# Performance work log

Measured on AMD Instinct MI355X. Metric: run time of the kernel, lower is better.

Reference implementation:

```python
import jax, jax.numpy as jnp
import numpy as np

B, T, V, E, U = 1024, 256, 50000, 512, 1024

def setup_inputs() -> dict:
    key = jax.random.key(0)
    ks = jax.random.split(key, 10)
    s = lambda k, shape, fan: jax.random.normal(k, shape, dtype=jnp.float32) * (1.0 / np.sqrt(fan))
    return {
        "inputs": jax.random.randint(ks[0], (B, T), 0, V, dtype=jnp.int32),
        "emb": s(ks[1], (V, E), E),
        "W0": s(ks[2], (E, U), E),
        "U0": s(ks[3], (U, U), U),
        "b0": jnp.zeros((U,), jnp.float32),
        "W1": s(ks[4], (U, U), U),
        "U1": s(ks[5], (U, U), U),
        "b1": jnp.zeros((U,), jnp.float32),
        "Wout": s(ks[6], (U, 1), U),
        "bout": jnp.zeros((1,), jnp.float32),
    }

def reference(inputs, emb, W0, U0, b0, W1, U1, b1, Wout, bout):
    x = emb[inputs]                      # [B, T, E] embedding lookup
    xT = jnp.swapaxes(x, 0, 1)           # [T, B, E] time-major for scan
    h0_init = jnp.zeros((inputs.shape[0], U0.shape[0]), x.dtype)
    h1_init = jnp.zeros((inputs.shape[0], U1.shape[0]), x.dtype)

    def step(carry, xt):
        h0, h1 = carry
        h0 = jnp.tanh(xt @ W0 + h0 @ U0 + b0)   # SimpleRNNCell 0 (dropout inactive, inference)
        h1 = jnp.tanh(h0 @ W1 + h1 @ U1 + b1)   # SimpleRNNCell 1
        return (h0, h1), None

    (h0, h1), _ = jax.lax.scan(step, (h0_init, h1_init), xT)
    return jax.nn.sigmoid(h1 @ Wout + bout)      # [B, 1]
```

## Files before the change

kernel.cpp:

```cpp
#include <hip/hip_runtime.h>
#include <hip/hip_cooperative_groups.h>
#include <math.h>

namespace cg = cooperative_groups;

typedef unsigned short u16;
typedef __bf16 bf16x8 __attribute__((ext_vector_type(8)));
typedef float f32x4 __attribute__((ext_vector_type(4)));
typedef unsigned short u16x8 __attribute__((ext_vector_type(8)));
typedef int i32x4 __attribute__((ext_vector_type(4)));

#define NBLK 256
#define NTHR 256
#define BB 1024
#define TT 256
#define EE 512
#define UU 1024
#define K0 1536
#define K1 2048
#define NK0 48
#define NK1 64
#define KTL0 32
#define KTL1 16
#define HN0 ((size_t)BB * K0)
#define HN1 ((size_t)BB * K1)
#define LDS_BYTES 163840

#define ROSTER_BASE 0
#define FLAG_BASE 32
#define EPOCH_BASE (32 + 2048)
#define BAR_INTS 2560

#define AUX_SC0 1

__device__ i32x4 llvm_amdgcn_raw_buffer_load_i32x4(i32x4 srsrc, int voffset, int soffset,
                                                   int aux) __asm("llvm.amdgcn.raw.buffer.load.v4i32");

__device__ __forceinline__ i32x4 make_srd(const void* p) {
  union { const void* p; int i[2]; } u; u.p = p;
  i32x4 r; r.x = u.i[0]; r.y = u.i[1]; r.z = -1; r.w = 0x00020000;
  return r;
}

__device__ __forceinline__ u16 f2bf(float f) {
  unsigned u = __builtin_bit_cast(unsigned, f);
  u += 0x7fffu + ((u >> 16) & 1u);
  return (u16)(u >> 16);
}
__device__ __forceinline__ float bf2f(u16 h) {
  return __builtin_bit_cast(float, ((unsigned)h) << 16);
}
__device__ __forceinline__ float fast_tanh(float x) {
  x = fminf(fmaxf(x, -15.f), 15.f);
  float e = __expf(2.f * x);
  return (e - 1.f) / (e + 1.f);
}

template<int K, int KLOW>
__device__ __forceinline__ void wfill(u16* __restrict__ Wt,
    const float* __restrict__ Wl, const float* __restrict__ Wh, int gstart) {
  constexpr int NK = K / 32;
  constexpr int NG = 1024 * K / 8;
  for (int g = gstart; g < NG; g += NBLK * NTHR) {
    const int lane = g & 63;
    const int r = g >> 6;
    const int kt = r % NK;
    const int cb = r / NK;
    const int n = cb * 16 + (lane & 15);
    const int kb = kt * 32 + (lane >> 4) * 8;
    u16x8 o;
#pragma unroll
    for (int e = 0; e < 8; ++e) {
      const int k = kb + e;
      const float v = (k < KLOW) ? Wl[(size_t)k * UU + n] : Wh[(size_t)(k - KLOW) * UU + n];
      o[e] = f2bf(v);
    }
    *(u16x8*)(Wt + (size_t)g * 8) = o;
  }
}

__device__ __forceinline__ void xbar(int* __restrict__ bar, int xcc, int slot, int nx,
                                     int tgt, int tid) {
  __syncthreads();
  if (tid < 64) {
    if (tid == 0)
      __hip_atomic_store(&bar[FLAG_BASE + xcc * 256 + slot], tgt,
                         __ATOMIC_RELAXED, __HIP_MEMORY_SCOPE_AGENT);
    if (slot == 0) {
      for (int base = 0; base < nx; base += 64) {
        const int i = base + tid;
        const bool act = (i < nx);
        int guard = 0;
        bool done = false;
        do {
          int v = act ? __hip_atomic_load(&bar[FLAG_BASE + xcc * 256 + i],
                                          __ATOMIC_RELAXED, __HIP_MEMORY_SCOPE_AGENT)
                      : tgt;
          done = __all(v >= tgt) != 0;
        } while (!done && ++guard < 300000);
      }
      if (tid == 0)
        __hip_atomic_store(&bar[EPOCH_BASE + xcc * 32], tgt,
                           __ATOMIC_RELAXED, __HIP_MEMORY_SCOPE_AGENT);
    } else if (tid == 0) {
      int guard = 0;
      while (__hip_atomic_load(&bar[EPOCH_BASE + xcc * 32],
                               __ATOMIC_RELAXED, __HIP_MEMORY_SCOPE_AGENT) < tgt
             && ++guard < 600000)
        __builtin_amdgcn_s_sleep(8);
    }
  }
  __syncthreads();
}

template<int K>
__device__ __forceinline__ void kstep(const i32x4& srdA, int voA, int kt,
    const u16* __restrict__ p0, const u16* __restrict__ p1,
    const u16* __restrict__ p2, const u16* __restrict__ p3,
    int lo, f32x4 (&acc)[2][4]) {
  i32x4 a0 = llvm_amdgcn_raw_buffer_load_i32x4(srdA, voA + kt * 64, 0, AUX_SC0);
  i32x4 a1 = llvm_amdgcn_raw_buffer_load_i32x4(srdA, voA + 16 * K * 2 + kt * 64, 0, AUX_SC0);
  u16x8 b0 = *(const u16x8*)(p0 + (size_t)kt * 512 + lo);
  u16x8 b1 = *(const u16x8*)(p1 + (size_t)kt * 512 + lo);
  u16x8 b2 = *(const u16x8*)(p2 + (size_t)kt * 512 + lo);
  u16x8 b3 = *(const u16x8*)(p3 + (size_t)kt * 512 + lo);
  bf16x8 fa0 = __builtin_bit_cast(bf16x8, a0);
  bf16x8 fa1 = __builtin_bit_cast(bf16x8, a1);
  bf16x8 fb0 = __builtin_bit_cast(bf16x8, b0);
  bf16x8 fb1 = __builtin_bit_cast(bf16x8, b1);
  bf16x8 fb2 = __builtin_bit_cast(bf16x8, b2);
  bf16x8 fb3 = __builtin_bit_cast(bf16x8, b3);
  acc[0][0] = __builtin_amdgcn_mfma_f32_16x16x32_bf16(fa0, fb0, acc[0][0], 0, 0, 0);
  acc[0][1] = __builtin_amdgcn_mfma_f32_16x16x32_bf16(fa0, fb1, acc[0][1], 0, 0, 0);
  acc[0][2] = __builtin_amdgcn_mfma_f32_16x16x32_bf16(fa0, fb2, acc[0][2], 0, 0, 0);
  acc[0][3] = __builtin_amdgcn_mfma_f32_16x16x32_bf16(fa0, fb3, acc[0][3], 0, 0, 0);
  acc[1][0] = __builtin_amdgcn_mfma_f32_16x16x32_bf16(fa1, fb0, acc[1][0], 0, 0, 0);
  acc[1][1] = __builtin_amdgcn_mfma_f32_16x16x32_bf16(fa1, fb1, acc[1][1], 0, 0, 0);
  acc[1][2] = __builtin_amdgcn_mfma_f32_16x16x32_bf16(fa1, fb2, acc[1][2], 0, 0, 0);
  acc[1][3] = __builtin_amdgcn_mfma_f32_16x16x32_bf16(fa1, fb3, acc[1][3], 0, 0, 0);
}

template<int K, int KTL>
__device__ __forceinline__ void gemm2(const i32x4& srdA, int voA,
    const u16* __restrict__ bA, const u16* __restrict__ bB,
    const u16* __restrict__ bP, int lane, f32x4 (&acc)[2][4]) {
  constexpr int NK = K / 32;
  const int lo = lane * 8;
  const u16* p0 = bA;
  const u16* p1 = bA + (size_t)NK * 512;
#pragma unroll 8
  for (int kt = 0; kt < KTL; ++kt)
    kstep<K>(srdA, voA, kt, p0, p1, bP, bP + (size_t)KTL * 512, lo, acc);
#pragma unroll 8
  for (int kt = KTL; kt < NK; ++kt)
    kstep<K>(srdA, voA, kt, p0, p1, bB, bB + (size_t)NK * 512, lo, acc);
}

__device__ __forceinline__ void do_l0(int tk, int xcc, int jl, bool uselds,
    const u16* __restrict__ ldsb, const u16* __restrict__ Wt0,
    const int* __restrict__ inputs, const float* __restrict__ emb,
    const float* __restrict__ b0, u16* __restrict__ A0, u16* __restrict__ A1,
    int tid)
{
  const int lane = tid & 63, w = tid >> 6, q = lane >> 4, l16 = lane & 15;
  const int c0 = jl * 64;
  if (tk < TT - 1) {
    const int grow = xcc * 128 + jl * 8 + (tid >> 5);
    const int c = (tid & 31) * 16;
    const int idx = inputs[grow * TT + tk + 1];
    const f32x4* s = (const f32x4*)(emb + (size_t)idx * EE + c);
    f32x4 f0 = s[0], f1 = s[1], f2 = s[2], f3 = s[3];
    u16x8 oa, ob;
#pragma unroll
    for (int j = 0; j < 4; ++j) {
      oa[j] = f2bf(f0[j]); oa[j + 4] = f2bf(f1[j]);
      ob[j] = f2bf(f2[j]); ob[j + 4] = f2bf(f3[j]);
    }
    u16* dst = A0 + (size_t)((tk + 1) & 1) * HN0 + (size_t)grow * K0 + c;
    *(u16x8*)dst = oa;
    *(u16x8*)(dst + 8) = ob;
  }
  if (tk < TT) {
    f32x4 acc[2][4];
#pragma unroll
    for (int i = 0; i < 2; ++i)
#pragma unroll
      for (int n = 0; n < 4; ++n) acc[i][n] = (f32x4){0.f, 0.f, 0.f, 0.f};
    i32x4 srdA = make_srd(A0 + (size_t)(tk & 1) * HN0);
    const int voA = ((xcc * 128 + w * 32 + l16) * K0 + q * 8) * 2;
    const u16* gA = Wt0 + (size_t)(c0 / 16) * NK0 * 512;
    const u16* bB = Wt0 + (size_t)(c0 / 16 + 2) * NK0 * 512;
    if (uselds) gemm2<K0, KTL0>(srdA, voA, ldsb, bB,
                                ldsb + (size_t)2 * NK0 * 512, lane, acc);
    else        gemm2<K0, 0   >(srdA, voA, gA, bB, ldsb, lane, acc);
    u16* d1 = A1 + (size_t)(tk & 1) * HN1;
    u16* d2 = A0 + (size_t)((tk + 1) & 1) * HN0 + 512;
#pragma unroll
    for (int n = 0; n < 4; ++n) {
      const int col = c0 + n * 16 + l16;
      const float bs = b0[col];
#pragma unroll
      for (int i = 0; i < 2; ++i) {
#pragma unroll
        for (int rr = 0; rr < 4; ++rr) {
          const int grow = xcc * 128 + w * 32 + i * 16 + q * 4 + rr;
          const u16 v = f2bf(fast_tanh(acc[i][n][rr] + bs));
          d1[(size_t)grow * K1 + col] = v;
          d2[(size_t)grow * K0 + col] = v;
        }
      }
    }
  }
}

__device__ __forceinline__ void do_l1(int tk, int xcc, int jl, bool uselds,
    const u16* __restrict__ ldsb, const u16* __restrict__ Wt1,
    const float* __restrict__ b1, u16* __restrict__ A1, int tid)
{
  const int lane = tid & 63, w = tid >> 6, q = lane >> 4, l16 = lane & 15;
  const int c0 = jl * 64;
  f32x4 acc[2][4];
#pragma unroll
  for (int i = 0; i < 2; ++i)
#pragma unroll
    for (int n = 0; n < 4; ++n) acc[i][n] = (f32x4){0.f, 0.f, 0.f, 0.f};
  i32x4 srdA = make_srd(A1 + (size_t)((tk - 1) & 1) * HN1);
  const int voA = ((xcc * 128 + w * 32 + l16) * K1 + q * 8) * 2;
  const u16* gA = Wt1 + (size_t)(c0 / 16) * NK1 * 512;
  const u16* bB = Wt1 + (size_t)(c0 / 16 + 2) * NK1 * 512;
  if (uselds) gemm2<K1, KTL1>(srdA, voA, ldsb, bB,
                              ldsb + (size_t)2 * NK1 * 512, lane, acc);
  else        gemm2<K1, 0   >(srdA, voA, gA, bB, ldsb, lane, acc);
  u16* d1 = A1 + (size_t)(tk & 1) * HN1 + 1024;
#pragma unroll
  for (int n = 0; n < 4; ++n) {
    const int col = c0 + n * 16 + l16;
    const float bs = b1[col];
#pragma unroll
    for (int i = 0; i < 2; ++i) {
#pragma unroll
      for (int rr = 0; rr < 4; ++rr) {
        const int grow = xcc * 128 + w * 32 + i * 16 + q * 4 + rr;
        d1[(size_t)grow * K1 + col] = f2bf(fast_tanh(acc[i][n][rr] + bs));
      }
    }
  }
}

__global__ __launch_bounds__(NTHR, 1)
void rnn_kernel(const int* __restrict__ inputs, const float* __restrict__ emb,
    const float* __restrict__ W0, const float* __restrict__ U0, const float* __restrict__ b0,
    const float* __restrict__ W1, const float* __restrict__ U1, const float* __restrict__ b1,
    const float* __restrict__ Wout, const float* __restrict__ bout,
    float* __restrict__ out,
    u16* __restrict__ Wt0, u16* __restrict__ Wt1,
    u16* __restrict__ A0, u16* __restrict__ A1, int* __restrict__ bar)
{
  extern __shared__ u16 lds[];
  int* li = (int*)lds;
  cg::grid_group grid = cg::this_grid();
  const int tid = threadIdx.x, bid = blockIdx.x;

  const int gstart = bid * NTHR + tid;
  wfill<K0, 512>(Wt0, W0, U0, gstart);
  wfill<K1, 1024>(Wt1, W1, U1, gstart);
  for (int g = gstart; g < BB * EE / 8; g += NBLK * NTHR) {
    const int b = g >> 6, seg = g & 63;
    const int idx = inputs[b * TT];
    const f32x4* s = (const f32x4*)(emb + (size_t)idx * EE + seg * 8);
    f32x4 f0 = s[0], f1 = s[1];
    u16x8 o;
#pragma unroll
    for (int j = 0; j < 4; ++j) { o[j] = f2bf(f0[j]); o[j + 4] = f2bf(f1[j]); }
    *(u16x8*)(A0 + (size_t)b * K0 + seg * 8) = o;
  }
  {
    const u16x8 z = {0, 0, 0, 0, 0, 0, 0, 0};
    for (int g = gstart; g < BB * 1024 / 8; g += NBLK * NTHR) {
      const int b = g >> 7, seg = g & 127;
      *(u16x8*)(A0 + (size_t)b * K0 + 512 + seg * 8) = z;
      *(u16x8*)(A1 + (size_t)b * K1 + 1024 + seg * 8) = z;
    }
  }
  if (bid == 0) for (int i = tid; i < BAR_INTS; i += NTHR) bar[i] = 0;
  grid.sync();

  if (tid == 0) {
    const int xc = __builtin_amdgcn_s_getreg((7 << 11) | 20) & 7;
    li[0] = xc;
    li[1] = atomicAdd(&bar[ROSTER_BASE + xc], 1);
  }
  __syncthreads();
  const int xcc = li[0], slot = li[1];
  __syncthreads();
  grid.sync();
  if (tid == 0)
    li[0] = __hip_atomic_load(&bar[ROSTER_BASE + xcc],
                              __ATOMIC_RELAXED, __HIP_MEMORY_SCOPE_AGENT);
  __syncthreads();
  const int nx = li[0];
  __syncthreads();

  if (slot < 32) {
    const bool pL0 = slot < 16;
    const int cb = (pL0 ? slot : slot - 16) * 4;
    const int NKp = pL0 ? NK0 : NK1;
    const int KTLp = pL0 ? KTL0 : KTL1;
    const u16* W = pL0 ? Wt0 : Wt1;
    const u16x8* s = (const u16x8*)(W + (size_t)cb * NKp * 512);
    const int nv = 2 * NKp * 64;
    u16x8* d = (u16x8*)lds;
    for (int i = tid; i < nv; i += NTHR) d[i] = s[i];
    u16x8* d2 = d + nv;
    const int nv2 = 2 * KTLp * 64;
    for (int i = tid; i < nv2; i += NTHR) {
      const int f = i / (KTLp * 64);
      const int rem = i - f * (KTLp * 64);
      d2[i] = *((const u16x8*)(W + (size_t)(cb + 2 + f) * NKp * 512) + rem);
    }
  }
  __syncthreads();

  for (int tk = 0; tk <= TT; ++tk) {
    for (int job = slot; job < 32; job += nx) {
      const bool uselds = (job == slot);
      if (job < 16) do_l0(tk, xcc, job, uselds, lds, Wt0, inputs, emb, b0, A0, A1, tid);
      else if (tk >= 1) do_l1(tk, xcc, job - 16, uselds, lds, Wt1, b1, A1, tid);
    }
    xbar(bar, xcc, slot, nx, tk + 1, tid);
  }

  if (slot == 0) {
    const int lane = tid & 63, w = tid >> 6;
    i32x4 srdH = make_srd(A1);
    const f32x4* wv = (const f32x4*)(Wout + lane * 16);
    f32x4 w0 = wv[0], w1 = wv[1], w2 = wv[2], w3 = wv[3];
    for (int rr = 0; rr < 32; ++rr) {
      const int grow = xcc * 128 + w * 32 + rr;
      const int vo = (grow * K1 + 1024 + lane * 16) * 2;
      i32x4 hv0 = llvm_amdgcn_raw_buffer_load_i32x4(srdH, vo, 0, AUX_SC0);
      i32x4 hv1 = llvm_amdgcn_raw_buffer_load_i32x4(srdH, vo + 16, 0, AUX_SC0);
      u16x8 lo = __builtin_bit_cast(u16x8, hv0);
      u16x8 hi = __builtin_bit_cast(u16x8, hv1);
      float s = 0.f;
#pragma unroll
      for (int j = 0; j < 4; ++j) {
        s += bf2f(lo[j]) * w0[j];
        s += bf2f(lo[j + 4]) * w1[j];
        s += bf2f(hi[j]) * w2[j];
        s += bf2f(hi[j + 4]) * w3[j];
      }
#pragma unroll
      for (int off = 32; off > 0; off >>= 1) s += __shfl_down(s, off);
      if (lane == 0) out[grow] = 1.f / (1.f + expf(-(s + bout[0])));
    }
  }
}

extern "C" void kernel_launch(void* const* d_in, const int* in_sizes, int n_in,
                              void* d_out, int out_size, void* d_ws, size_t ws_size,
                              hipStream_t stream)
{
  (void)in_sizes; (void)n_in; (void)out_size; (void)ws_size;
  const int*   inputs = (const int*)d_in[0];
  const float* emb    = (const float*)d_in[1];
  const float* W0     = (const float*)d_in[2];
  const float* U0     = (const float*)d_in[3];
  const float* b0     = (const float*)d_in[4];
  const float* W1     = (const float*)d_in[5];
  const float* U1     = (const float*)d_in[6];
  const float* b1     = (const float*)d_in[7];
  const float* Wout   = (const float*)d_in[8];
  const float* bout   = (const float*)d_in[9];
  float* out = (float*)d_out;

  u16* Wt0 = (u16*)d_ws;
  u16* Wt1 = Wt0 + (size_t)1024 * K0;
  u16* A0  = Wt1 + (size_t)1024 * K1;
  u16* A1  = A0 + (size_t)2 * 1024 * K0;
  int* bar = (int*)(A1 + (size_t)2 * 1024 * K1);

  static int lds_set = 0;
  if (!lds_set) {
    hipFuncSetAttribute((const void*)rnn_kernel,
                        hipFuncAttributeMaxDynamicSharedMemorySize, LDS_BYTES);
    lds_set = 1;
  }

  void* args[] = { &inputs, &emb, &W0, &U0, &b0, &W1, &U1, &b1, &Wout, &bout,
                   &out, &Wt0, &Wt1, &A0, &A1, &bar };
  hipLaunchCooperativeKernel((void*)rnn_kernel, dim3(NBLK), dim3(NTHR), args, LDS_BYTES, stream);
}
```

Measured before the change: 7.214 ms.

## Double block threads to 512, each wave computing 16 rows instead of 32

Raises the block size from 256 to 512 threads, so each of 8 waves computes a 16-row by 64-column tile instead of a 32x64 tile. The A-fragment load and half the MFMAs per k-step move to the extra waves, and the embedding staging and output reduction are reindexed to match. This raises per-CU wave parallelism and latency hiding for the per-timestep GEMMs. The cost is that each B fragment, read from LDS or global memory, is now loaded by twice as many waves for half as much reuse, and register pressure per wave changes under launch_bounds(512,1).

```diff
diff --git a/kernel.cpp b/kernel.cpp
--- a/kernel.cpp
+++ b/kernel.cpp
@@ -11,7 +11,7 @@
 typedef int i32x4 __attribute__((ext_vector_type(4)));
 
 #define NBLK 256
-#define NTHR 256
+#define NTHR 512
 #define BB 1024
 #define TT 256
 #define EE 512
@@ -117,33 +117,27 @@
 __device__ __forceinline__ void kstep(const i32x4& srdA, int voA, int kt,
     const u16* __restrict__ p0, const u16* __restrict__ p1,
     const u16* __restrict__ p2, const u16* __restrict__ p3,
-    int lo, f32x4 (&acc)[2][4]) {
+    int lo, f32x4 (&acc)[4]) {
   i32x4 a0 = llvm_amdgcn_raw_buffer_load_i32x4(srdA, voA + kt * 64, 0, AUX_SC0);
-  i32x4 a1 = llvm_amdgcn_raw_buffer_load_i32x4(srdA, voA + 16 * K * 2 + kt * 64, 0, AUX_SC0);
   u16x8 b0 = *(const u16x8*)(p0 + (size_t)kt * 512 + lo);
   u16x8 b1 = *(const u16x8*)(p1 + (size_t)kt * 512 + lo);
   u16x8 b2 = *(const u16x8*)(p2 + (size_t)kt * 512 + lo);
   u16x8 b3 = *(const u16x8*)(p3 + (size_t)kt * 512 + lo);
   bf16x8 fa0 = __builtin_bit_cast(bf16x8, a0);
-  bf16x8 fa1 = __builtin_bit_cast(bf16x8, a1);
   bf16x8 fb0 = __builtin_bit_cast(bf16x8, b0);
   bf16x8 fb1 = __builtin_bit_cast(bf16x8, b1);
   bf16x8 fb2 = __builtin_bit_cast(bf16x8, b2);
   bf16x8 fb3 = __builtin_bit_cast(bf16x8, b3);
-  acc[0][0] = __builtin_amdgcn_mfma_f32_16x16x32_bf16(fa0, fb0, acc[0][0], 0, 0, 0);
-  acc[0][1] = __builtin_amdgcn_mfma_f32_16x16x32_bf16(fa0, fb1, acc[0][1], 0, 0, 0);
-  acc[0][2] = __builtin_amdgcn_mfma_f32_16x16x32_bf16(fa0, fb2, acc[0][2], 0, 0, 0);
-  acc[0][3] = __builtin_amdgcn_mfma_f32_16x16x32_bf16(fa0, fb3, acc[0][3], 0, 0, 0);
-  acc[1][0] = __builtin_amdgcn_mfma_f32_16x16x32_bf16(fa1, fb0, acc[1][0], 0, 0, 0);
-  acc[1][1] = __builtin_amdgcn_mfma_f32_16x16x32_bf16(fa1, fb1, acc[1][1], 0, 0, 0);
-  acc[1][2] = __builtin_amdgcn_mfma_f32_16x16x32_bf16(fa1, fb2, acc[1][2], 0, 0, 0);
-  acc[1][3] = __builtin_amdgcn_mfma_f32_16x16x32_bf16(fa1, fb3, acc[1][3], 0, 0, 0);
+  acc[0] = __builtin_amdgcn_mfma_f32_16x16x32_bf16(fa0, fb0, acc[0], 0, 0, 0);
+  acc[1] = __builtin_amdgcn_mfma_f32_16x16x32_bf16(fa0, fb1, acc[1], 0, 0, 0);
+  acc[2] = __builtin_amdgcn_mfma_f32_16x16x32_bf16(fa0, fb2, acc[2], 0, 0, 0);
+  acc[3] = __builtin_amdgcn_mfma_f32_16x16x32_bf16(fa0, fb3, acc[3], 0, 0, 0);
 }
 
 template<int K, int KTL>
 __device__ __forceinline__ void gemm2(const i32x4& srdA, int voA,
     const u16* __restrict__ bA, const u16* __restrict__ bB,
-    const u16* __restrict__ bP, int lane, f32x4 (&acc)[2][4]) {
+    const u16* __restrict__ bP, int lane, f32x4 (&acc)[4]) {
   constexpr int NK = K / 32;
   const int lo = lane * 8;
   const u16* p0 = bA;
@@ -165,29 +159,22 @@
   const int lane = tid & 63, w = tid >> 6, q = lane >> 4, l16 = lane & 15;
   const int c0 = jl * 64;
   if (tk < TT - 1) {
-    const int grow = xcc * 128 + jl * 8 + (tid >> 5);
-    const int c = (tid & 31) * 16;
+    const int grow = xcc * 128 + jl * 8 + (tid >> 6);
+    const int c = (tid & 63) * 8;
     const int idx = inputs[grow * TT + tk + 1];
     const f32x4* s = (const f32x4*)(emb + (size_t)idx * EE + c);
-    f32x4 f0 = s[0], f1 = s[1], f2 = s[2], f3 = s[3];
-    u16x8 oa, ob;
-#pragma unroll
-    for (int j = 0; j < 4; ++j) {
-      oa[j] = f2bf(f0[j]); oa[j + 4] = f2bf(f1[j]);
-      ob[j] = f2bf(f2[j]); ob[j + 4] = f2bf(f3[j]);
-    }
-    u16* dst = A0 + (size_t)((tk + 1) & 1) * HN0 + (size_t)grow * K0 + c;
-    *(u16x8*)dst = oa;
-    *(u16x8*)(dst + 8) = ob;
+    f32x4 f0 = s[0], f1 = s[1];
+    u16x8 oa;
+#pragma unroll
+    for (int j = 0; j < 4; ++j) { oa[j] = f2bf(f0[j]); oa[j + 4] = f2bf(f1[j]); }
+    *(u16x8*)(A0 + (size_t)((tk + 1) & 1) * HN0 + (size_t)grow * K0 + c) = oa;
   }
   if (tk < TT) {
-    f32x4 acc[2][4];
-#pragma unroll
-    for (int i = 0; i < 2; ++i)
-#pragma unroll
-      for (int n = 0; n < 4; ++n) acc[i][n] = (f32x4){0.f, 0.f, 0.f, 0.f};
+    f32x4 acc[4];
+#pragma unroll
+    for (int n = 0; n < 4; ++n) acc[n] = (f32x4){0.f, 0.f, 0.f, 0.f};
     i32x4 srdA = make_srd(A0 + (size_t)(tk & 1) * HN0);
-    const int voA = ((xcc * 128 + w * 32 + l16) * K0 + q * 8) * 2;
+    const int voA = ((xcc * 128 + w * 16 + l16) * K0 + q * 8) * 2;
     const u16* gA = Wt0 + (size_t)(c0 / 16) * NK0 * 512;
     const u16* bB = Wt0 + (size_t)(c0 / 16 + 2) * NK0 * 512;
     if (uselds) gemm2<K0, KTL0>(srdA, voA, ldsb, bB,
@@ -200,14 +187,11 @@
       const int col = c0 + n * 16 + l16;
       const float bs = b0[col];
 #pragma unroll
-      for (int i = 0; i < 2; ++i) {
-#pragma unroll
-        for (int rr = 0; rr < 4; ++rr) {
-          const int grow = xcc * 128 + w * 32 + i * 16 + q * 4 + rr;
-          const u16 v = f2bf(fast_tanh(acc[i][n][rr] + bs));
-          d1[(size_t)grow * K1 + col] = v;
-          d2[(size_t)grow * K0 + col] = v;
-        }
+      for (int rr = 0; rr < 4; ++rr) {
+        const int grow = xcc * 128 + w * 16 + q * 4 + rr;
+        const u16 v = f2bf(fast_tanh(acc[n][rr] + bs));
+        d1[(size_t)grow * K1 + col] = v;
+        d2[(size_t)grow * K0 + col] = v;
       }
     }
   }
@@ -219,13 +203,11 @@
 {
   const int lane = tid & 63, w = tid >> 6, q = lane >> 4, l16 = lane & 15;
   const int c0 = jl * 64;
-  f32x4 acc[2][4];
-#pragma unroll
-  for (int i = 0; i < 2; ++i)
-#pragma unroll
-    for (int n = 0; n < 4; ++n) acc[i][n] = (f32x4){0.f, 0.f, 0.f, 0.f};
+  f32x4 acc[4];
+#pragma unroll
+  for (int n = 0; n < 4; ++n) acc[n] = (f32x4){0.f, 0.f, 0.f, 0.f};
   i32x4 srdA = make_srd(A1 + (size_t)((tk - 1) & 1) * HN1);
-  const int voA = ((xcc * 128 + w * 32 + l16) * K1 + q * 8) * 2;
+  const int voA = ((xcc * 128 + w * 16 + l16) * K1 + q * 8) * 2;
   const u16* gA = Wt1 + (size_t)(c0 / 16) * NK1 * 512;
   const u16* bB = Wt1 + (size_t)(c0 / 16 + 2) * NK1 * 512;
   if (uselds) gemm2<K1, KTL1>(srdA, voA, ldsb, bB,
@@ -237,12 +219,9 @@
     const int col = c0 + n * 16 + l16;
     const float bs = b1[col];
 #pragma unroll
-    for (int i = 0; i < 2; ++i) {
-#pragma unroll
-      for (int rr = 0; rr < 4; ++rr) {
-        const int grow = xcc * 128 + w * 32 + i * 16 + q * 4 + rr;
-        d1[(size_t)grow * K1 + col] = f2bf(fast_tanh(acc[i][n][rr] + bs));
-      }
+    for (int rr = 0; rr < 4; ++rr) {
+      const int grow = xcc * 128 + w * 16 + q * 4 + rr;
+      d1[(size_t)grow * K1 + col] = f2bf(fast_tanh(acc[n][rr] + bs));
     }
   }
 }
@@ -335,8 +314,8 @@
     i32x4 srdH = make_srd(A1);
     const f32x4* wv = (const f32x4*)(Wout + lane * 16);
     f32x4 w0 = wv[0], w1 = wv[1], w2 = wv[2], w3 = wv[3];
-    for (int rr = 0; rr < 32; ++rr) {
-      const int grow = xcc * 128 + w * 32 + rr;
+    for (int rr = 0; rr < 16; ++rr) {
+      const int grow = xcc * 128 + w * 16 + rr;
       const int vo = (grow * K1 + 1024 + lane * 16) * 2;
       i32x4 hv0 = llvm_amdgcn_raw_buffer_load_i32x4(srdH, vo, 0, AUX_SC0);
       i32x4 hv1 = llvm_amdgcn_raw_buffer_load_i32x4(srdH, vo + 16, 0, AUX_SC0);
```

New measurement: 6.403 ms. 11.2% less time.
